# Performance work log

Measured on AMD Instinct MI355X. Metric: run time of the kernel, lower is better.

The kernel has to match this reference:

```python
import jax, jax.numpy as jnp
import numpy as np

EMBED = 64
HEADS = 2
HDIM = EMBED // HEADS  # 32
IN_FEAT = 256
NODES = 3


def _lin(x, W, b=None):
    y = x @ W.T
    return y + b if b is not None else y


def setup_inputs() -> dict:
    key = jax.random.key(0)
    ks = jax.random.split(key, 24)
    B = 131072
    s = 0.05
    inp = {
        "spatial": jax.random.normal(ks[0], (B, IN_FEAT), jnp.float32),
        "genomic": jax.random.normal(ks[1], (B, IN_FEAT), jnp.float32),
        "temporal": jax.random.normal(ks[2], (B, IN_FEAT), jnp.float32),
        "adj_matrix": jnp.ones((B, NODES, NODES), jnp.float32),
        # modality projections (Linear(256,64))
        "Wsp": jax.random.normal(ks[3], (EMBED, IN_FEAT)) * s,
        "bsp": jnp.zeros((EMBED,)),
        "Wge": jax.random.normal(ks[4], (EMBED, IN_FEAT)) * s,
        "bge": jnp.zeros((EMBED,)),
        "Wtm": jax.random.normal(ks[5], (EMBED, IN_FEAT)) * s,
        "btm": jnp.zeros((EMBED,)),
        # GAT: W Linear(64,64,no bias), attention Linear(2*head_dim=64 -> 1, no bias)
        "gat_W": jax.random.normal(ks[6], (EMBED, EMBED)) * s,
        "gat_a": jax.random.normal(ks[7], (2 * HDIM,)) * s,
        # MultiheadAttention(64, 2)
        "in_w": jax.random.normal(ks[8], (3 * EMBED, EMBED)) * s,
        "in_b": jnp.zeros((3 * EMBED,)),
        "out_w": jax.random.normal(ks[9], (EMBED, EMBED)) * s,
        "out_b": jnp.zeros((EMBED,)),
        # LayerNorm(64)
        "ln_g": jnp.ones((EMBED,)),
        "ln_b": jnp.zeros((EMBED,)),
        # predictor 64->32->16->2
        "p1_w": jax.random.normal(ks[10], (32, EMBED)) * s,
        "p1_b": jnp.zeros((32,)),
        "p2_w": jax.random.normal(ks[11], (16, 32)) * s,
        "p2_b": jnp.zeros((16,)),
        "p3_w": jax.random.normal(ks[12], (2, 16)) * s,
        "p3_b": jnp.zeros((2,)),
    }
    return inp


def reference(spatial, genomic, temporal, adj_matrix,
              Wsp, bsp, Wge, bge, Wtm, btm,
              gat_W, gat_a, in_w, in_b, out_w, out_b,
              ln_g, ln_b, p1_w, p1_b, p2_w, p2_b, p3_w, p3_b):
    # Dropout layers are identity in eval mode.
    B = spatial.shape[0]
    sp = jax.nn.relu(_lin(spatial, Wsp, bsp))   # [B, 64]
    ge = jax.nn.relu(_lin(genomic, Wge, bge))
    tm = jax.nn.relu(_lin(temporal, Wtm, btm))
    x = jnp.stack([sp, ge, tm], axis=1)          # [B, 3, 64]

    # ---- GAT layer (dense attention over 3 nodes, 2 heads) ----
    h = _lin(x, gat_W).reshape(B, NODES, HEADS, HDIM)  # [B,3,H,D]
    # a . concat(h_i, h_j) decomposes into a1.h_i + a2.h_j
    e_i = jnp.einsum('bnhd,d->bnh', h, gat_a[:HDIM])
    e_j = jnp.einsum('bnhd,d->bnh', h, gat_a[HDIM:])
    e = e_i[:, :, None, :] + e_j[:, None, :, :]        # [B,3,3,H]
    e = jnp.where(e > 0, e, 0.2 * e)                    # LeakyReLU(0.2)
    e = jnp.where(adj_matrix[..., None] == 0, -1e9, e)
    alpha = jax.nn.softmax(e, axis=2)                   # softmax over j
    h_out = jnp.einsum('bijh,bjhd->bihd', alpha, h).reshape(B, NODES, EMBED)
    gat_pooled = h_out.mean(axis=1)                     # [B, 64]

    # ---- Cross-modal MHA + residual LayerNorm ----
    qkv = _lin(x, in_w, in_b)                           # [B,3,192]
    q, k, v = jnp.split(qkv, 3, axis=-1)
    def heads(t):
        return t.reshape(B, NODES, HEADS, HDIM).transpose(0, 2, 1, 3)
    q, k, v = heads(q), heads(k), heads(v)              # [B,H,3,D]
    sc = jnp.einsum('bhqd,bhkd->bhqk', q, k) / jnp.sqrt(jnp.float32(HDIM))
    attn = jax.nn.softmax(sc, axis=-1)
    o = jnp.einsum('bhqk,bhkd->bhqd', attn, v).transpose(0, 2, 1, 3).reshape(B, NODES, EMBED)
    attn_out = _lin(o, out_w, out_b)
    y = x + attn_out
    mu = y.mean(-1, keepdims=True)
    var = ((y - mu) ** 2).mean(-1, keepdims=True)
    y = (y - mu) / jnp.sqrt(var + 1e-5) * ln_g + ln_b
    cross_modal = y.mean(axis=1)                        # [B, 64]

    # ---- Predictor ----
    combined = gat_pooled + cross_modal
    z = jax.nn.relu(_lin(combined, p1_w, p1_b))
    z = jax.nn.relu(_lin(z, p2_w, p2_b))
    out = _lin(z, p3_w, p3_b)                           # [B, 2]
    return out[:, 0], out[:, 1]
```

## Files before the change

kernel.cpp:

```cpp
#include <hip/hip_runtime.h>

typedef __attribute__((ext_vector_type(8))) short v8s;
typedef __attribute__((ext_vector_type(4))) float v4f;

#define MFMA16(a, b, c) __builtin_amdgcn_mfma_f32_16x16x32_bf16((a), (b), (c), 0, 0, 0)
#define SCQ 0.17677669529663687f

__device__ __forceinline__ short f2bf(float f) {
    unsigned u = __float_as_uint(f);
    u += 0x7FFFu + ((u >> 16) & 1u);
    return (short)(u >> 16);
}
__device__ __forceinline__ float bf2f(short s) {
    return __uint_as_float(((unsigned)(unsigned short)s) << 16);
}
__device__ __forceinline__ float bfly16(float v) {
#pragma unroll
    for (int m = 1; m < 16; m <<= 1) v += __shfl_xor(v, m);
    return v;
}

__global__ void giman_prep(const float* __restrict__ Wsp, const float* __restrict__ Wge,
                           const float* __restrict__ Wtm, const float* __restrict__ gatW,
                           const float* __restrict__ gat_a,
                           const float* __restrict__ inw, const float* __restrict__ outw,
                           const float* __restrict__ p1w, const float* __restrict__ p2w,
                           const float* __restrict__ in_b, const float* __restrict__ out_b,
                           short* __restrict__ ws) {
    int idx = blockIdx.x * 256 + threadIdx.x;
    if (idx < 73216) {
        int j = idx & 7, l = (idx >> 3) & 63;
        int lr = l & 15, lc = ((l >> 4) << 3) + j;
        float val;
        if (idx < 49152) {
            const float* W; int off;
            if (idx < 16384)      { W = Wsp; off = idx; }
            else if (idx < 32768) { W = Wge; off = idx - 16384; }
            else                  { W = Wtm; off = idx - 32768; }
            int t = off >> 9, kk = t & 7, nb = t >> 3;
            val = W[(nb * 16 + lr) * 256 + kk * 32 + lc];
        } else if (idx < 54272) {
            int t = (idx - 49152) >> 9, kk = t & 1, nb = t >> 1;
            if (nb < 4) {
                val = gatW[(nb * 16 + lr) * 64 + kk * 32 + lc];
            } else {
                val = 0.f;
                if (lr < 4) {
                    int f = kk * 32 + lc;
                    float s = 0.f;
                    for (int d = 0; d < 32; ++d)
                        s += gat_a[(lr >> 1) * 32 + d] * gatW[((lr & 1) * 32 + d) * 64 + f];
                    val = s;
                }
            }
        } else if (idx < 62464) {
            int t = (idx - 54272) >> 9, kk = t & 1, nb = t >> 1;
            int row = nb * 16 + lr;
            val = inw[row * 64 + kk * 32 + lc] * (row < 64 ? SCQ : 1.f);
        } else if (idx < 70656) {
            int t = (idx - 62464) >> 9, kk = t & 1, nbh = t >> 1;
            int h = nbh >> 2, nb = nbh & 3;
            int r = nb * 16 + lr, c = kk * 32 + lc;
            float s = 0.f;
            for (int k = 0; k < 32; ++k)
                s += outw[r * 64 + h * 32 + k] * inw[(128 + h * 32 + k) * 64 + c];
            val = s;
        } else if (idx < 72704) {
            int t = (idx - 70656) >> 9, kk = t & 1, nb = t >> 1;
            val = p1w[(nb * 16 + lr) * 64 + kk * 32 + lc];
        } else {
            val = p2w[lr * 32 + lc];
        }
        ws[idx] = f2bf(val);
    } else if (idx < 73280) {
        int r = idx - 73216;
        float s = out_b[r];
        for (int k = 0; k < 64; ++k) s += outw[r * 64 + 128 + k] * in_b[128 + k];
        ((float*)(ws + 73216))[r] = s;
    }
}

__global__ __launch_bounds__(256)
void giman_main(const float* __restrict__ spatial, const float* __restrict__ genomic,
                const float* __restrict__ temporal, const float* __restrict__ adj,
                const short* __restrict__ wf,
                const float* __restrict__ bsp, const float* __restrict__ bge,
                const float* __restrict__ btm,
                const float* __restrict__ in_b, const float* __restrict__ ln_g,
                const float* __restrict__ ln_b, const float* __restrict__ p1b,
                const float* __restrict__ p2b, const float* __restrict__ p3w,
                const float* __restrict__ p3bb,
                float* __restrict__ dout, int Btot)
{
    __shared__ __align__(16) short x_lds[4][48][72];
    __shared__ __align__(16) short c_lds[4][16][72];
    __shared__ __align__(16) short q_tr[4][16][72];
    __shared__ __align__(16) short k_tr[4][16][72];
    __shared__ __align__(16) float a_lds[4][148];

    const int wv   = threadIdx.x >> 6;
    const int lane = threadIdx.x & 63;
    const int lq   = lane & 15;
    const int lg   = lane >> 4;
    const int grpb = lane & 48;
    const int s0   = blockIdx.x * 64 + wv * 16;
    if (s0 + 16 > Btot) return;

    short (*xw)[72] = x_lds[wv];
    short (*qtr)[72] = q_tr[wv];
    short (*ktr)[72] = k_tr[wv];

    if (lane < 36)
        *(float4*)&a_lds[wv][lane * 4] = *(const float4*)(adj + (size_t)s0 * 9 + lane * 4);

#pragma unroll
    for (int nb = 0; nb < 4; ++nb) {
        qtr[lg * 4 + 3][nb * 16 + lq] = 0;
        ktr[lg * 4 + 3][nb * 16 + lq] = 0;
    }

    const float* cbp = (const float*)(wf + 73216);
    float cbv[4], lgv[4], lbv[4], ibv[8];
#pragma unroll
    for (int nb = 0; nb < 4; ++nb) {
        int c = nb * 16 + lq;
        cbv[nb] = cbp[c];
        lgv[nb] = ln_g[c];
        lbv[nb] = ln_b[c];
    }
#pragma unroll
    for (int nb = 0; nb < 8; ++nb)
        ibv[nb] = in_b[nb * 16 + lq] * (nb < 4 ? SCQ : 1.f);
    const float inv3 = 1.f / 3.f;

    {
        const float* Xs[3] = {spatial, genomic, temporal};
        const float* Bs[3] = {bsp, bge, btm};
#pragma unroll
        for (int m = 0; m < 3; ++m) {
            const float* X = Xs[m] + (size_t)(s0 + lq) * 256 + lg * 8;
            const v8s* bwf = (const v8s*)(wf + m * 16384);
            v4f acc[4];
#pragma unroll
            for (int nb = 0; nb < 4; ++nb) acc[nb] = (v4f){0.f, 0.f, 0.f, 0.f};
#pragma unroll 4
            for (int kk = 0; kk < 8; ++kk) {
                float4 u = *(const float4*)(X + kk * 32);
                float4 v = *(const float4*)(X + kk * 32 + 4);
                v8s af;
                af[0] = f2bf(u.x); af[1] = f2bf(u.y); af[2] = f2bf(u.z); af[3] = f2bf(u.w);
                af[4] = f2bf(v.x); af[5] = f2bf(v.y); af[6] = f2bf(v.z); af[7] = f2bf(v.w);
#pragma unroll
                for (int nb = 0; nb < 4; ++nb)
                    acc[nb] = MFMA16(af, bwf[(nb * 8 + kk) * 64 + lane], acc[nb]);
            }
#pragma unroll
            for (int nb = 0; nb < 4; ++nb) {
                float bb = Bs[m][nb * 16 + lq];
#pragma unroll
                for (int r = 0; r < 4; ++r) {
                    float v = acc[nb][r] + bb;
                    v = v > 0.f ? v : 0.f;
                    xw[(lg * 4 + r) * 3 + m][nb * 16 + lq] = f2bf(v);
                }
            }
        }
    }

    const v8s* gwf = (const v8s*)(wf + 49152);
    const v8s* qkf = (const v8s*)(wf + 54272);
    const v8s* uf  = (const v8s*)(wf + 62464);

#pragma unroll 1
    for (int t = 0; t < 4; ++t) {
        int rn = lq & 3; rn = (rn == 3) ? 2 : rn;
        const short* xrp = xw[(t * 4 + (lq >> 2)) * 3 + rn];
        v8s xa0 = *(const v8s*)(xrp + lg * 8);
        v8s xa1 = *(const v8s*)(xrp + 32 + lg * 8);

        float gp[4];
        {
            v4f hacc[4];
#pragma unroll
            for (int nb = 0; nb < 4; ++nb) {
                v4f a = (v4f){0.f, 0.f, 0.f, 0.f};
                a = MFMA16(xa0, gwf[(nb * 2 + 0) * 64 + lane], a);
                a = MFMA16(xa1, gwf[(nb * 2 + 1) * 64 + lane], a);
                hacc[nb] = a;
            }
            v4f eacc = (v4f){0.f, 0.f, 0.f, 0.f};
            eacc = MFMA16(xa0, gwf[8 * 64 + lane], eacc);
            eacc = MFMA16(xa1, gwf[9 * 64 + lane], eacc);

            float eiv[3][2], ejv[3][2];
#pragma unroll
            for (int r = 0; r < 3; ++r) {
#pragma unroll
                for (int h = 0; h < 2; ++h) {
                    eiv[r][h] = __shfl(eacc[r], grpb + h);
                    ejv[r][h] = __shfl(eacc[r], grpb + 2 + h);
                }
            }

            const float* amp = &a_lds[wv][(t * 4 + lg) * 9];
            float wj0[2] = {}, wj1[2] = {}, wj2[2] = {};
#pragma unroll
            for (int h = 0; h < 2; ++h)
#pragma unroll
                for (int i = 0; i < 3; ++i) {
                    float e0 = eiv[i][h] + ejv[0][h]; e0 = e0 > 0.f ? e0 : 0.2f * e0; if (amp[i * 3 + 0] == 0.f) e0 = -1e9f;
                    float e1 = eiv[i][h] + ejv[1][h]; e1 = e1 > 0.f ? e1 : 0.2f * e1; if (amp[i * 3 + 1] == 0.f) e1 = -1e9f;
                    float e2 = eiv[i][h] + ejv[2][h]; e2 = e2 > 0.f ? e2 : 0.2f * e2; if (amp[i * 3 + 2] == 0.f) e2 = -1e9f;
                    float mx = fmaxf(e0, fmaxf(e1, e2));
                    float q0 = __expf(e0 - mx), q1 = __expf(e1 - mx), q2 = __expf(e2 - mx);
                    float inv = 1.f / (q0 + q1 + q2);
                    wj0[h] += q0 * inv; wj1[h] += q1 * inv; wj2[h] += q2 * inv;
                }
#pragma unroll
            for (int nb = 0; nb < 4; ++nb) {
                int h = nb >> 1;
                gp[nb] = (wj0[h] * hacc[nb][0] + wj1[h] * hacc[nb][1] + wj2[h] * hacc[nb][2]) * inv3;
            }
        }

        {
            v4f qa[4], ka[4];
#pragma unroll
            for (int nb = 0; nb < 4; ++nb) {
                float bb = ibv[nb];
                v4f a = (v4f){bb, bb, bb, bb};
                a = MFMA16(xa0, qkf[(nb * 2 + 0) * 64 + lane], a);
                a = MFMA16(xa1, qkf[(nb * 2 + 1) * 64 + lane], a);
                qa[nb] = a;
            }
#pragma unroll
            for (int nb = 0; nb < 4; ++nb) {
                float bb = ibv[4 + nb];
                v4f a = (v4f){bb, bb, bb, bb};
                a = MFMA16(xa0, qkf[((4 + nb) * 2 + 0) * 64 + lane], a);
                a = MFMA16(xa1, qkf[((4 + nb) * 2 + 1) * 64 + lane], a);
                ka[nb] = a;
            }
#pragma unroll
            for (int nb = 0; nb < 4; ++nb)
#pragma unroll
                for (int r = 0; r < 3; ++r) {
                    qtr[lg * 4 + r][nb * 16 + lq] = f2bf(qa[nb][r]);
                    ktr[lg * 4 + r][nb * 16 + lq] = f2bf(ka[nb][r]);
                }
        }

        float al[2][9];
        {
            const int sb = grpb + (grpb >> 2);
#pragma unroll
            for (int h = 0; h < 2; ++h) {
                v8s aq = *(const v8s*)&qtr[lq][h * 32 + lg * 8];
                v8s bk = *(const v8s*)&ktr[lq][h * 32 + lg * 8];
                v4f S = (v4f){0.f, 0.f, 0.f, 0.f};
                S = MFMA16(aq, bk, S);
                float sc[9];
#pragma unroll
                for (int i = 0; i < 3; ++i)
#pragma unroll
                    for (int j = 0; j < 3; ++j)
                        sc[i * 3 + j] = __shfl(S[i], sb + j);
#pragma unroll
                for (int i = 0; i < 3; ++i) {
                    float e0 = sc[i * 3 + 0], e1 = sc[i * 3 + 1], e2 = sc[i * 3 + 2];
                    float mx = fmaxf(e0, fmaxf(e1, e2));
                    float w0 = __expf(e0 - mx), w1 = __expf(e1 - mx), w2 = __expf(e2 - mx);
                    float inv = 1.f / (w0 + w1 + w2);
                    al[h][i * 3 + 0] = w0 * inv;
                    al[h][i * 3 + 1] = w1 * inv;
                    al[h][i * 3 + 2] = w2 * inv;
                }
            }
        }

        float y[4][3];
#pragma unroll
        for (int nb = 0; nb < 4; ++nb)
#pragma unroll
            for (int r = 0; r < 3; ++r)
                y[nb][r] = bf2f(xw[(t * 4 + lg) * 3 + r][nb * 16 + lq]) + cbv[nb];
#pragma unroll
        for (int h = 0; h < 2; ++h)
#pragma unroll
            for (int nb = 0; nb < 4; ++nb) {
                v4f u = (v4f){0.f, 0.f, 0.f, 0.f};
                u = MFMA16(xa0, uf[((h * 4 + nb) * 2 + 0) * 64 + lane], u);
                u = MFMA16(xa1, uf[((h * 4 + nb) * 2 + 1) * 64 + lane], u);
#pragma unroll
                for (int r = 0; r < 3; ++r)
                    y[nb][r] += al[h][r * 3 + 0] * u[0] + al[h][r * 3 + 1] * u[1]
                              + al[h][r * 3 + 2] * u[2];
            }

        float mu[3], rs[3];
#pragma unroll
        for (int r = 0; r < 3; ++r) {
            float sm = y[0][r] + y[1][r] + y[2][r] + y[3][r];
            float sq = y[0][r] * y[0][r] + y[1][r] * y[1][r]
                     + y[2][r] * y[2][r] + y[3][r] * y[3][r];
            sm = bfly16(sm); sq = bfly16(sq);
            float m_ = sm * (1.f / 64.f);
            float var = sq * (1.f / 64.f) - m_ * m_;
            mu[r] = m_;
            rs[r] = rsqrtf(var + 1e-5f);
        }
#pragma unroll
        for (int nb = 0; nb < 4; ++nb) {
            float cm = (y[nb][0] - mu[0]) * rs[0] + (y[nb][1] - mu[1]) * rs[1]
                     + (y[nb][2] - mu[2]) * rs[2];
            float comb = gp[nb] + cm * inv3 * lgv[nb] + lbv[nb];
            c_lds[wv][t * 4 + lg][nb * 16 + lq] = f2bf(comb);
        }
    }

    {
        const v8s* p1f = (const v8s*)(wf + 70656);
        const v8s* p2f = (const v8s*)(wf + 72704);
        short (*zw)[40] = (short (*)[40])(&x_lds[wv][0][0]);
        const short* crp = &c_lds[wv][lq][0];
        v8s ca0 = *(const v8s*)(crp + lg * 8);
        v8s ca1 = *(const v8s*)(crp + 32 + lg * 8);
        const float pb1v0 = p1b[lq], pb1v1 = p1b[16 + lq], pb2v = p2b[lq];
        const float p3w0 = p3w[lq], p3w1 = p3w[16 + lq];
        v4f z1[2];
#pragma unroll
        for (int nb = 0; nb < 2; ++nb) {
            float bb = nb ? pb1v1 : pb1v0;
            v4f a = (v4f){bb, bb, bb, bb};
            a = MFMA16(ca0, p1f[(nb * 2 + 0) * 64 + lane], a);
            a = MFMA16(ca1, p1f[(nb * 2 + 1) * 64 + lane], a);
            z1[nb] = a;
        }
#pragma unroll
        for (int nb = 0; nb < 2; ++nb)
#pragma unroll
            for (int r = 0; r < 4; ++r) {
                float v = z1[nb][r];
                v = v > 0.f ? v : 0.f;
                zw[lg * 4 + r][nb * 16 + lq] = f2bf(v);
            }
        v8s za = *(const v8s*)(&zw[lq][0] + lg * 8);
        v4f z2 = (v4f){pb2v, pb2v, pb2v, pb2v};
        z2 = MFMA16(za, p2f[lane], z2);
        const float p3b0 = p3bb[0], p3b1 = p3bb[1];
#pragma unroll
        for (int r = 0; r < 4; ++r) {
            float v = z2[r];
            v = v > 0.f ? v : 0.f;
            float po0 = bfly16(v * p3w0);
            float po1 = bfly16(v * p3w1);
            if (lq == 0) {
                dout[s0 + lg * 4 + r] = po0 + p3b0;
                dout[Btot + s0 + lg * 4 + r] = po1 + p3b1;
            }
        }
    }
}

extern "C" void kernel_launch(void* const* d_in, const int* in_sizes, int n_in,
                              void* d_out, int out_size, void* d_ws, size_t ws_size,
                              hipStream_t stream) {
    const float* spatial  = (const float*)d_in[0];
    const float* genomic  = (const float*)d_in[1];
    const float* temporal = (const float*)d_in[2];
    const float* adj      = (const float*)d_in[3];
    const float* Wsp = (const float*)d_in[4];
    const float* bsp = (const float*)d_in[5];
    const float* Wge = (const float*)d_in[6];
    const float* bge = (const float*)d_in[7];
    const float* Wtm = (const float*)d_in[8];
    const float* btm = (const float*)d_in[9];
    const float* gatW  = (const float*)d_in[10];
    const float* gat_a = (const float*)d_in[11];
    const float* in_w  = (const float*)d_in[12];
    const float* in_b  = (const float*)d_in[13];
    const float* out_w = (const float*)d_in[14];
    const float* out_b = (const float*)d_in[15];
    const float* ln_g  = (const float*)d_in[16];
    const float* ln_b  = (const float*)d_in[17];
    const float* p1w = (const float*)d_in[18];
    const float* p1b = (const float*)d_in[19];
    const float* p2w = (const float*)d_in[20];
    const float* p2b = (const float*)d_in[21];
    const float* p3w = (const float*)d_in[22];
    const float* p3b = (const float*)d_in[23];
    float* out = (float*)d_out;
    const int Btot = in_sizes[0] / 256;

    short* wf = (short*)d_ws;

    giman_prep<<<(73280 + 255) / 256, 256, 0, stream>>>(Wsp, Wge, Wtm, gatW, gat_a,
                                                        in_w, out_w, p1w, p2w,
                                                        in_b, out_b, wf);
    giman_main<<<Btot / 64, 256, 0, stream>>>(spatial, genomic, temporal, adj, wf,
                                              bsp, bge, btm, in_b,
                                              ln_g, ln_b, p1b, p2b, p3w, p3b,
                                              out, Btot);
}
```

Measured before the change: 207.7 us.

## Fold Wq^T Wk into precomputed bilinear weight and drop separate Q/K projections

Attention scores are now computed as x_i^T (Wq_h^T Wk_h) x_j, with the combined 64x64 bilinear matrix per head (scaled) precomputed in the prep kernel. Bias cross-terms are folded into extra columns of the GAT logit weight and a scalar constant, so the main kernel no longer builds Q and K tiles or keeps their LDS buffers. LDS use drops, the combined buffer reuses x_lds, and launch bounds now request 4 blocks per SM with a smaller unroll, aiming for higher occupancy. The cost is an extra MFMA stage plus an LDS round trip per head, and more rounding because the folded product matrix is stored in bf16.

```diff
diff --git a/kernel.cpp b/kernel.cpp
--- a/kernel.cpp
+++ b/kernel.cpp
@@ -44,19 +44,35 @@
             if (nb < 4) {
                 val = gatW[(nb * 16 + lr) * 64 + kk * 32 + lc];
             } else {
+                int f = kk * 32 + lc;
                 val = 0.f;
                 if (lr < 4) {
-                    int f = kk * 32 + lc;
                     float s = 0.f;
                     for (int d = 0; d < 32; ++d)
                         s += gat_a[(lr >> 1) * 32 + d] * gatW[((lr & 1) * 32 + d) * 64 + f];
                     val = s;
+                } else if (lr < 6) {
+                    int h = lr - 4;
+                    float s = 0.f;
+                    for (int d = 0; d < 32; ++d)
+                        s += inw[(32 * h + d) * 64 + f] * in_b[64 + 32 * h + d];
+                    val = s * SCQ;
+                } else if (lr < 8) {
+                    int h = lr - 6;
+                    float s = 0.f;
+                    for (int d = 0; d < 32; ++d)
+                        s += inw[(64 + 32 * h + d) * 64 + f] * in_b[32 * h + d];
+                    val = s * SCQ;
                 }
             }
         } else if (idx < 62464) {
-            int t = (idx - 54272) >> 9, kk = t & 1, nb = t >> 1;
-            int row = nb * 16 + lr;
-            val = inw[row * 64 + kk * 32 + lc] * (row < 64 ? SCQ : 1.f);
+            int t = (idx - 54272) >> 9, kk = t & 1, nbh = t >> 1;
+            int h = nbh >> 2, nb = nbh & 3;
+            int a = kk * 32 + lc, b = nb * 16 + lr;
+            float s = 0.f;
+            for (int d = 0; d < 32; ++d)
+                s += inw[(32 * h + d) * 64 + a] * inw[(64 + 32 * h + d) * 64 + b];
+            val = s * SCQ;
         } else if (idx < 70656) {
             int t = (idx - 62464) >> 9, kk = t & 1, nbh = t >> 1;
             int h = nbh >> 2, nb = nbh & 3;
@@ -77,25 +93,27 @@
         float s = out_b[r];
         for (int k = 0; k < 64; ++k) s += outw[r * 64 + 128 + k] * in_b[128 + k];
         ((float*)(ws + 73216))[r] = s;
-    }
-}
-
-__global__ __launch_bounds__(256)
+    } else if (idx < 73282) {
+        int h = idx - 73280;
+        float s = 0.f;
+        for (int d = 0; d < 32; ++d) s += in_b[32 * h + d] * in_b[64 + 32 * h + d];
+        ((float*)(ws + 73216))[64 + h] = s * SCQ;
+    }
+}
+
+__global__ __launch_bounds__(256, 4)
 void giman_main(const float* __restrict__ spatial, const float* __restrict__ genomic,
                 const float* __restrict__ temporal, const float* __restrict__ adj,
                 const short* __restrict__ wf,
                 const float* __restrict__ bsp, const float* __restrict__ bge,
                 const float* __restrict__ btm,
-                const float* __restrict__ in_b, const float* __restrict__ ln_g,
-                const float* __restrict__ ln_b, const float* __restrict__ p1b,
-                const float* __restrict__ p2b, const float* __restrict__ p3w,
-                const float* __restrict__ p3bb,
+                const float* __restrict__ ln_g, const float* __restrict__ ln_b,
+                const float* __restrict__ p1b, const float* __restrict__ p2b,
+                const float* __restrict__ p3w, const float* __restrict__ p3bb,
                 float* __restrict__ dout, int Btot)
 {
     __shared__ __align__(16) short x_lds[4][48][72];
-    __shared__ __align__(16) short c_lds[4][16][72];
-    __shared__ __align__(16) short q_tr[4][16][72];
-    __shared__ __align__(16) short k_tr[4][16][72];
+    __shared__ __align__(16) short v_lds[4][16][72];
     __shared__ __align__(16) float a_lds[4][148];
 
     const int wv   = threadIdx.x >> 6;
@@ -107,20 +125,13 @@
     if (s0 + 16 > Btot) return;
 
     short (*xw)[72] = x_lds[wv];
-    short (*qtr)[72] = q_tr[wv];
-    short (*ktr)[72] = k_tr[wv];
+    short (*vtr)[72] = v_lds[wv];
 
     if (lane < 36)
         *(float4*)&a_lds[wv][lane * 4] = *(const float4*)(adj + (size_t)s0 * 9 + lane * 4);
 
-#pragma unroll
-    for (int nb = 0; nb < 4; ++nb) {
-        qtr[lg * 4 + 3][nb * 16 + lq] = 0;
-        ktr[lg * 4 + 3][nb * 16 + lq] = 0;
-    }
-
     const float* cbp = (const float*)(wf + 73216);
-    float cbv[4], lgv[4], lbv[4], ibv[8];
+    float cbv[4], lgv[4], lbv[4];
 #pragma unroll
     for (int nb = 0; nb < 4; ++nb) {
         int c = nb * 16 + lq;
@@ -128,9 +139,7 @@
         lgv[nb] = ln_g[c];
         lbv[nb] = ln_b[c];
     }
-#pragma unroll
-    for (int nb = 0; nb < 8; ++nb)
-        ibv[nb] = in_b[nb * 16 + lq] * (nb < 4 ? SCQ : 1.f);
+    const float gmv0 = cbp[64], gmv1 = cbp[65];
     const float inv3 = 1.f / 3.f;
 
     {
@@ -143,7 +152,7 @@
             v4f acc[4];
 #pragma unroll
             for (int nb = 0; nb < 4; ++nb) acc[nb] = (v4f){0.f, 0.f, 0.f, 0.f};
-#pragma unroll 4
+#pragma unroll 2
             for (int kk = 0; kk < 8; ++kk) {
                 float4 u = *(const float4*)(X + kk * 32);
                 float4 v = *(const float4*)(X + kk * 32 + 4);
@@ -168,7 +177,7 @@
     }
 
     const v8s* gwf = (const v8s*)(wf + 49152);
-    const v8s* qkf = (const v8s*)(wf + 54272);
+    const v8s* pff = (const v8s*)(wf + 54272);
     const v8s* uf  = (const v8s*)(wf + 62464);
 
 #pragma unroll 1
@@ -179,6 +188,7 @@
         v8s xa1 = *(const v8s*)(xrp + 32 + lg * 8);
 
         float gp[4];
+        float av[3][2], bv[3][2];
         {
             v4f hacc[4];
 #pragma unroll
@@ -194,13 +204,14 @@
 
             float eiv[3][2], ejv[3][2];
 #pragma unroll
-            for (int r = 0; r < 3; ++r) {
+            for (int r = 0; r < 3; ++r)
 #pragma unroll
                 for (int h = 0; h < 2; ++h) {
                     eiv[r][h] = __shfl(eacc[r], grpb + h);
                     ejv[r][h] = __shfl(eacc[r], grpb + 2 + h);
+                    av[r][h]  = __shfl(eacc[r], grpb + 4 + h);
+                    bv[r][h]  = __shfl(eacc[r], grpb + 6 + h) + (h ? gmv1 : gmv0);
                 }
-            }
 
             const float* amp = &a_lds[wv][(t * 4 + lg) * 9];
             float wj0[2] = {}, wj1[2] = {}, wj2[2] = {};
@@ -223,58 +234,41 @@
             }
         }
 
-        {
-            v4f qa[4], ka[4];
-#pragma unroll
-            for (int nb = 0; nb < 4; ++nb) {
-                float bb = ibv[nb];
-                v4f a = (v4f){bb, bb, bb, bb};
-                a = MFMA16(xa0, qkf[(nb * 2 + 0) * 64 + lane], a);
-                a = MFMA16(xa1, qkf[(nb * 2 + 1) * 64 + lane], a);
-                qa[nb] = a;
-            }
-#pragma unroll
-            for (int nb = 0; nb < 4; ++nb) {
-                float bb = ibv[4 + nb];
-                v4f a = (v4f){bb, bb, bb, bb};
-                a = MFMA16(xa0, qkf[((4 + nb) * 2 + 0) * 64 + lane], a);
-                a = MFMA16(xa1, qkf[((4 + nb) * 2 + 1) * 64 + lane], a);
-                ka[nb] = a;
+        float al[2][9];
+        const int sb = grpb + (grpb >> 2);
+#pragma unroll
+        for (int h = 0; h < 2; ++h) {
+            v4f va[4];
+#pragma unroll
+            for (int nb = 0; nb < 4; ++nb) {
+                v4f a = (v4f){0.f, 0.f, 0.f, 0.f};
+                a = MFMA16(xa0, pff[((h * 4 + nb) * 2 + 0) * 64 + lane], a);
+                a = MFMA16(xa1, pff[((h * 4 + nb) * 2 + 1) * 64 + lane], a);
+                va[nb] = a;
             }
 #pragma unroll
             for (int nb = 0; nb < 4; ++nb)
 #pragma unroll
-                for (int r = 0; r < 3; ++r) {
-                    qtr[lg * 4 + r][nb * 16 + lq] = f2bf(qa[nb][r]);
-                    ktr[lg * 4 + r][nb * 16 + lq] = f2bf(ka[nb][r]);
-                }
-        }
-
-        float al[2][9];
-        {
-            const int sb = grpb + (grpb >> 2);
-#pragma unroll
-            for (int h = 0; h < 2; ++h) {
-                v8s aq = *(const v8s*)&qtr[lq][h * 32 + lg * 8];
-                v8s bk = *(const v8s*)&ktr[lq][h * 32 + lg * 8];
-                v4f S = (v4f){0.f, 0.f, 0.f, 0.f};
-                S = MFMA16(aq, bk, S);
-                float sc[9];
-#pragma unroll
-                for (int i = 0; i < 3; ++i)
-#pragma unroll
-                    for (int j = 0; j < 3; ++j)
-                        sc[i * 3 + j] = __shfl(S[i], sb + j);
-#pragma unroll
-                for (int i = 0; i < 3; ++i) {
-                    float e0 = sc[i * 3 + 0], e1 = sc[i * 3 + 1], e2 = sc[i * 3 + 2];
-                    float mx = fmaxf(e0, fmaxf(e1, e2));
-                    float w0 = __expf(e0 - mx), w1 = __expf(e1 - mx), w2 = __expf(e2 - mx);
-                    float inv = 1.f / (w0 + w1 + w2);
-                    al[h][i * 3 + 0] = w0 * inv;
-                    al[h][i * 3 + 1] = w1 * inv;
-                    al[h][i * 3 + 2] = w2 * inv;
-                }
+                for (int r = 0; r < 3; ++r)
+                    vtr[lg * 4 + r][nb * 16 + lq] = f2bf(va[nb][r]);
+
+            v8s aq0 = *(const v8s*)&vtr[lq][lg * 8];
+            v8s aq1 = *(const v8s*)&vtr[lq][32 + lg * 8];
+            v4f S = (v4f){0.f, 0.f, 0.f, 0.f};
+            S = MFMA16(aq0, xa0, S);
+            S = MFMA16(aq1, xa1, S);
+
+#pragma unroll
+            for (int i = 0; i < 3; ++i) {
+                float e0 = __shfl(S[i], sb + 0) + av[i][h] + bv[0][h];
+                float e1 = __shfl(S[i], sb + 1) + av[i][h] + bv[1][h];
+                float e2 = __shfl(S[i], sb + 2) + av[i][h] + bv[2][h];
+                float mx = fmaxf(e0, fmaxf(e1, e2));
+                float w0 = __expf(e0 - mx), w1 = __expf(e1 - mx), w2 = __expf(e2 - mx);
+                float inv = 1.f / (w0 + w1 + w2);
+                al[h][i * 3 + 0] = w0 * inv;
+                al[h][i * 3 + 1] = w1 * inv;
+                al[h][i * 3 + 2] = w2 * inv;
             }
         }
 
@@ -314,15 +308,15 @@
             float cm = (y[nb][0] - mu[0]) * rs[0] + (y[nb][1] - mu[1]) * rs[1]
                      + (y[nb][2] - mu[2]) * rs[2];
             float comb = gp[nb] + cm * inv3 * lgv[nb] + lbv[nb];
-            c_lds[wv][t * 4 + lg][nb * 16 + lq] = f2bf(comb);
+            xw[t * 4 + lg][nb * 16 + lq] = f2bf(comb);
         }
     }
 
     {
         const v8s* p1f = (const v8s*)(wf + 70656);
         const v8s* p2f = (const v8s*)(wf + 72704);
-        short (*zw)[40] = (short (*)[40])(&x_lds[wv][0][0]);
-        const short* crp = &c_lds[wv][lq][0];
+        short (*zw)[40] = (short (*)[40])(&xw[16][0]);
+        const short* crp = &xw[lq][0];
         v8s ca0 = *(const v8s*)(crp + lg * 8);
         v8s ca1 = *(const v8s*)(crp + 32 + lg * 8);
         const float pb1v0 = p1b[lq], pb1v1 = p1b[16 + lq], pb2v = p2b[lq];
@@ -394,11 +388,11 @@
 
     short* wf = (short*)d_ws;
 
-    giman_prep<<<(73280 + 255) / 256, 256, 0, stream>>>(Wsp, Wge, Wtm, gatW, gat_a,
+    giman_prep<<<(73282 + 255) / 256, 256, 0, stream>>>(Wsp, Wge, Wtm, gatW, gat_a,
                                                         in_w, out_w, p1w, p2w,
                                                         in_b, out_b, wf);
     giman_main<<<Btot / 64, 256, 0, stream>>>(spatial, genomic, temporal, adj, wf,
-                                              bsp, bge, btm, in_b,
+                                              bsp, bge, btm,
                                               ln_g, ln_b, p1b, p2b, p3w, p3b,
                                               out, Btot);
 }
```

After: 361.4 us. +74.0%, slower.
